# Performance work log

Measured on AMD Instinct MI355X. Metric: run time of the kernel, lower is better.

## Reference

```python
import jax, jax.numpy as jnp
import numpy as np

EPS = 1.0


def _onedirectional_dist(a, b):
    # a: (B, M), b: (B, N) -> per-batch sum over M of min_n (a_m - b_n)^2
    d2 = (a[:, :, None] - b[:, None, :]) ** 2  # (B, M, N)
    return jnp.min(d2, axis=2).sum(axis=1)  # (B,)


def setup_inputs() -> dict:
    key = jax.random.key(0)
    k1, k2, k3 = jax.random.split(key, 3)
    target = jax.random.uniform(k1, (4, 240, 320), dtype=jnp.float32)
    bin_centers = jax.random.uniform(k2, (4, 256), dtype=jnp.float32)
    mask = jax.random.randint(k3, (4, 240, 320), 0, 2).astype(jnp.bool_)
    return {"target": target, "bin_centers": bin_centers, "mask": mask}


def reference(target, bin_centers, mask):
    # masked path of ChamferDistanceLoss.forward
    max_target = jnp.max(jnp.where(mask, target, -jnp.inf))
    max_center = jnp.max(bin_centers)
    mx = jnp.maximum(max_target, max_center)
    mn = jnp.minimum(max_target, max_center)
    pad_value = mx + (mx - mn) + EPS
    B = bin_centers.shape[0]
    # pad bin_centers with one extra column = pad_value
    mod_centers = jnp.concatenate(
        [bin_centers, jnp.broadcast_to(pad_value, (B, 1)).astype(bin_centers.dtype)],
        axis=1,
    )  # (B, n_bins + 1)
    # invalid target pixels replaced by pad_value
    mod_target = jnp.where(mask, target, pad_value).reshape(B, -1)  # (B, H*W)
    bidir = _onedirectional_dist(mod_centers, mod_target) + _onedirectional_dist(
        mod_target, mod_centers
    )
    return jnp.mean(bidir)
```

## Files before the change

### kernel.cpp

```cpp
#include <hip/hip_runtime.h>
#include <math.h>

#define B 4
#define HW 76800
#define NBINS 256
#define TPB 256
#define PXB 1024
#define BPB (HW / PXB)
#define NINT 257
#define KBUK 1024
#define PMW (B * BPB * NINT)
#define TPB2 1024


__device__ __forceinline__ unsigned umaxu(unsigned a, unsigned b) { return a > b ? a : b; }
__device__ __forceinline__ unsigned uminu(unsigned a, unsigned b) { return a < b ? a : b; }

__global__ __launch_bounds__(256) void kmain(const float* __restrict__ target,
                                             const int* __restrict__ mask,
                                             const float* __restrict__ centers,
                                             float* __restrict__ out,
                                             unsigned* __restrict__ ws) {
    __shared__ __align__(16) float s_ct[NBINS];
    __shared__ __align__(16) float s_sc[NBINS];
    __shared__ unsigned short s_tab[KBUK];
    __shared__ unsigned s_M[NINT];
    __shared__ unsigned s_m[NINT];
    __shared__ float s_red[4];
    const int tid = threadIdx.x;
    const int b   = blockIdx.y;
    const int blk = blockIdx.x;

    const float ci = centers[b * NBINS + tid];
    s_ct[tid] = ci;
    s_M[tid]  = 0u;
    s_m[tid]  = 0x7F800000u;
    if (tid == 0) { s_M[256] = 0u; s_m[256] = 0x7F800000u; }
    __syncthreads();

    int rank = 0;
    const float4* c4 = (const float4*)s_ct;
#pragma unroll 8
    for (int g = 0; g < NBINS / 4; ++g) {
        float4 c = c4[g];
        const int j0 = 4 * g;
        rank += (c.x < ci) || (c.x == ci && (j0 + 0) < tid);
        rank += (c.y < ci) || (c.y == ci && (j0 + 1) < tid);
        rank += (c.z < ci) || (c.z == ci && (j0 + 2) < tid);
        rank += (c.w < ci) || (c.w == ci && (j0 + 3) < tid);
    }
    s_sc[rank] = ci;
    __syncthreads();

    {
        const float cr = s_sc[tid];
        const int k0 = (int)(cr * (float)KBUK);
        const int k1 = (tid == NBINS - 1) ? (KBUK - 1)
                                          : (int)(s_sc[tid + 1] * (float)KBUK);
        for (int k = k0 + 1; k <= k1; ++k) s_tab[k] = (unsigned short)(tid + 1);
        if (tid == 0)
            for (int k = 0; k <= k0; ++k) s_tab[k] = 0;
    }
    __syncthreads();

    const int base = b * HW + blk * PXB;
    const float4 p4 = ((const float4*)(target + base))[tid];
    const int4   m4 = ((const int4*)(mask + base))[tid];
    float acc = 0.f;
#pragma unroll
    for (int c = 0; c < 4; ++c) {
        const float p = (c == 0) ? p4.x : (c == 1) ? p4.y : (c == 2) ? p4.z : p4.w;
        const int   m = (c == 0) ? m4.x : (c == 1) ? m4.y : (c == 2) ? m4.z : m4.w;
        int j = s_tab[(int)(p * (float)KBUK)];
        while (j < NBINS && s_sc[j] < p) ++j;
        const float dp = (j > 0)     ? (p - s_sc[j - 1]) : 3e38f;
        const float ds = (j < NBINS) ? (s_sc[j] - p)     : 3e38f;
        if (m) {
            acc += fminf(dp * dp, ds * ds);
            const unsigned pb = __float_as_uint(p);
            atomicMax(&s_M[j], pb);
            atomicMin(&s_m[j], pb);
        }
    }

    for (int o = 32; o > 0; o >>= 1) acc += __shfl_down(acc, o);
    if ((tid & 63) == 0) s_red[tid >> 6] = acc;
    __syncthreads();
    if (tid == 0)
        atomicAdd(out, 0.25f * (s_red[0] + s_red[1] + s_red[2] + s_red[3]));

    unsigned* pM = ws + (size_t)(b * BPB + blk) * NINT;
    unsigned* pm = ws + (size_t)PMW + (size_t)(b * BPB + blk) * NINT;
    pM[tid] = s_M[tid];
    pm[tid] = s_m[tid];
    if (tid == 0) { pM[256] = s_M[256]; pm[256] = s_m[256]; }
}

__global__ __launch_bounds__(1024) void kfold(const float* __restrict__ centers,
                                              const unsigned* __restrict__ ws,
                                              float* __restrict__ out) {
    __shared__ __align__(16) float s_ct[NBINS];
    __shared__ __align__(16) float s_sc[NBINS];
    __shared__ unsigned s_Mp[NINT * 4];
    __shared__ unsigned s_mp[NINT * 4];
    __shared__ float s_P[512];
    __shared__ float s_S[512];
    __shared__ float s_red[4];
    const int tid = threadIdx.x;
    const int b   = blockIdx.x;

    if (tid < NBINS) s_ct[tid] = centers[b * NBINS + tid];
    __syncthreads();
    if (tid < NBINS) {
        const float ci = s_ct[tid];
        int rank = 0;
        const float4* c4 = (const float4*)s_ct;
#pragma unroll 8
        for (int g = 0; g < NBINS / 4; ++g) {
            float4 c = c4[g];
            const int j0 = 4 * g;
            rank += (c.x < ci) || (c.x == ci && (j0 + 0) < tid);
            rank += (c.y < ci) || (c.y == ci && (j0 + 1) < tid);
            rank += (c.z < ci) || (c.z == ci && (j0 + 2) < tid);
            rank += (c.w < ci) || (c.w == ci && (j0 + 3) < tid);
        }
        s_sc[rank] = ci;
    }

    const unsigned* pM = ws + (size_t)b * BPB * NINT;
    const unsigned* pm = ws + (size_t)PMW + (size_t)b * BPB * NINT;
    for (int idx = tid; idx < NINT * 4; idx += TPB2) {
        const int j = idx >> 2, q = idx & 3;
        const int k0 = (q * BPB) / 4, k1 = ((q + 1) * BPB) / 4;
        unsigned Mb = 0u, mb = 0x7F800000u;
        for (int k = k0; k < k1; ++k) {
            Mb = umaxu(Mb, pM[(size_t)k * NINT + j]);
            mb = uminu(mb, pm[(size_t)k * NINT + j]);
        }
        s_Mp[idx] = Mb;
        s_mp[idx] = mb;
    }
    __syncthreads();

    if (tid < 512) {
        if (tid < NINT) {
            unsigned Mb = umaxu(umaxu(s_Mp[4 * tid], s_Mp[4 * tid + 1]),
                                umaxu(s_Mp[4 * tid + 2], s_Mp[4 * tid + 3]));
            unsigned mb = uminu(uminu(s_mp[4 * tid], s_mp[4 * tid + 1]),
                                uminu(s_mp[4 * tid + 2], s_mp[4 * tid + 3]));
            const bool empty = (Mb == 0u) && (mb == 0x7F800000u);
            s_P[tid] = empty ? -3e38f : __uint_as_float(Mb);
            s_S[tid] = empty ?  3e38f : __uint_as_float(mb);
        } else {
            s_P[tid] = -3e38f;
            s_S[tid] =  3e38f;
        }
    }
    __syncthreads();

    for (int s = 1; s < 512; s <<= 1) {
        float pa = 0.f, sa = 0.f;
        if (tid < 512) {
            pa = fmaxf(s_P[tid], (tid >= s) ? s_P[tid - s] : -3e38f);
            sa = fminf(s_S[tid], (tid + s < 512) ? s_S[tid + s] : 3e38f);
        }
        __syncthreads();
        if (tid < 512) { s_P[tid] = pa; s_S[tid] = sa; }
        __syncthreads();
    }

    float d1 = 0.f;
    if (tid < NBINS) {
        const float c = s_sc[tid];
        const float a = c - s_P[tid];
        const float d = s_S[tid + 1] - c;
        d1 = fminf(a * a, d * d);
    }
    for (int o = 32; o > 0; o >>= 1) d1 += __shfl_down(d1, o);
    if ((tid & 63) == 0 && tid < NBINS) s_red[tid >> 6] = d1;
    __syncthreads();
    if (tid == 0)
        atomicAdd(out, 0.25f * (s_red[0] + s_red[1] + s_red[2] + s_red[3]));
}

extern "C" void kernel_launch(void* const* d_in, const int* in_sizes, int n_in,
                              void* d_out, int out_size, void* d_ws, size_t ws_size,
                              hipStream_t stream) {
    const float* target  = (const float*)d_in[0];
    const float* centers = (const float*)d_in[1];
    const int*   mask    = (const int*)d_in[2];
    float* out = (float*)d_out;

    dim3 g1(BPB, B);
    kmain<<<g1, TPB, 0, stream>>>(target, mask, centers, out, (unsigned*)d_ws);
    kfold<<<dim3(B), TPB2, 0, stream>>>(centers, (const unsigned*)d_ws, out);
}
```

Measured before the change: 87.25 us.

## Fuse main and fold kernels into one cooperative launch with grid sync

Merges the per-block histogram kernel and the per-batch fold kernel into a single cooperative kernel that uses a grid-wide sync before one block per batch performs the fold. The fold's parallel Hillis-Steele prefix scan is replaced by a serial per-thread running max/min over the sorted intervals, and the cross-block reduction now runs over all blocks in one pass per thread. This removes a second kernel launch and its dispatch gap, but adds grid-sync overhead across 300 blocks and leaves the fold on four blocks of 256 threads, so it does less parallel work than the 1024-thread fold it replaces.

```diff
diff --git a/kernel.cpp b/kernel.cpp
--- a/kernel.cpp
+++ b/kernel.cpp
@@ -1,5 +1,8 @@
 #include <hip/hip_runtime.h>
+#include <hip/hip_cooperative_groups.h>
 #include <math.h>
+
+namespace cg = cooperative_groups;
 
 #define B 4
 #define HW 76800
@@ -10,22 +13,23 @@
 #define NINT 257
 #define KBUK 1024
 #define PMW (B * BPB * NINT)
-#define TPB2 1024
 
 
 __device__ __forceinline__ unsigned umaxu(unsigned a, unsigned b) { return a > b ? a : b; }
 __device__ __forceinline__ unsigned uminu(unsigned a, unsigned b) { return a < b ? a : b; }
 
-__global__ __launch_bounds__(256) void kmain(const float* __restrict__ target,
-                                             const int* __restrict__ mask,
-                                             const float* __restrict__ centers,
-                                             float* __restrict__ out,
-                                             unsigned* __restrict__ ws) {
+__global__ __launch_bounds__(256) void kchamfer(const float* __restrict__ target,
+                                                const int* __restrict__ mask,
+                                                const float* __restrict__ centers,
+                                                float* __restrict__ out,
+                                                unsigned* __restrict__ ws) {
     __shared__ __align__(16) float s_ct[NBINS];
     __shared__ __align__(16) float s_sc[NBINS];
     __shared__ unsigned short s_tab[KBUK];
     __shared__ unsigned s_M[NINT];
     __shared__ unsigned s_m[NINT];
+    __shared__ float s_P[NINT];
+    __shared__ float s_S[NINT];
     __shared__ float s_red[4];
     const int tid = threadIdx.x;
     const int b   = blockIdx.y;
@@ -94,90 +98,46 @@
     pM[tid] = s_M[tid];
     pm[tid] = s_m[tid];
     if (tid == 0) { pM[256] = s_M[256]; pm[256] = s_m[256]; }
-}
 
-__global__ __launch_bounds__(1024) void kfold(const float* __restrict__ centers,
-                                              const unsigned* __restrict__ ws,
-                                              float* __restrict__ out) {
-    __shared__ __align__(16) float s_ct[NBINS];
-    __shared__ __align__(16) float s_sc[NBINS];
-    __shared__ unsigned s_Mp[NINT * 4];
-    __shared__ unsigned s_mp[NINT * 4];
-    __shared__ float s_P[512];
-    __shared__ float s_S[512];
-    __shared__ float s_red[4];
-    const int tid = threadIdx.x;
-    const int b   = blockIdx.x;
+    __threadfence();
+    cg::this_grid().sync();
+    __threadfence();
 
-    if (tid < NBINS) s_ct[tid] = centers[b * NBINS + tid];
-    __syncthreads();
-    if (tid < NBINS) {
-        const float ci = s_ct[tid];
-        int rank = 0;
-        const float4* c4 = (const float4*)s_ct;
-#pragma unroll 8
-        for (int g = 0; g < NBINS / 4; ++g) {
-            float4 c = c4[g];
-            const int j0 = 4 * g;
-            rank += (c.x < ci) || (c.x == ci && (j0 + 0) < tid);
-            rank += (c.y < ci) || (c.y == ci && (j0 + 1) < tid);
-            rank += (c.z < ci) || (c.z == ci && (j0 + 2) < tid);
-            rank += (c.w < ci) || (c.w == ci && (j0 + 3) < tid);
+    if (blk != 0) return;
+
+    const unsigned* gM = ws + (size_t)b * BPB * NINT;
+    const unsigned* gm = ws + (size_t)PMW + (size_t)b * BPB * NINT;
+    for (int j = tid; j < NINT; j += TPB) {
+        unsigned Mb = 0u, mb = 0x7F800000u;
+#pragma unroll 5
+        for (int k = 0; k < BPB; ++k) {
+            Mb = umaxu(Mb, gM[(size_t)k * NINT + j]);
+            mb = uminu(mb, gm[(size_t)k * NINT + j]);
         }
-        s_sc[rank] = ci;
-    }
-
-    const unsigned* pM = ws + (size_t)b * BPB * NINT;
-    const unsigned* pm = ws + (size_t)PMW + (size_t)b * BPB * NINT;
-    for (int idx = tid; idx < NINT * 4; idx += TPB2) {
-        const int j = idx >> 2, q = idx & 3;
-        const int k0 = (q * BPB) / 4, k1 = ((q + 1) * BPB) / 4;
-        unsigned Mb = 0u, mb = 0x7F800000u;
-        for (int k = k0; k < k1; ++k) {
-            Mb = umaxu(Mb, pM[(size_t)k * NINT + j]);
-            mb = uminu(mb, pm[(size_t)k * NINT + j]);
-        }
-        s_Mp[idx] = Mb;
-        s_mp[idx] = mb;
+        const bool empty = (Mb == 0u) && (mb == 0x7F800000u);
+        s_P[j] = empty ? -3e38f : __uint_as_float(Mb);
+        s_S[j] = empty ?  3e38f : __uint_as_float(mb);
     }
     __syncthreads();
 
-    if (tid < 512) {
-        if (tid < NINT) {
-            unsigned Mb = umaxu(umaxu(s_Mp[4 * tid], s_Mp[4 * tid + 1]),
-                                umaxu(s_Mp[4 * tid + 2], s_Mp[4 * tid + 3]));
-            unsigned mb = uminu(uminu(s_mp[4 * tid], s_mp[4 * tid + 1]),
-                                uminu(s_mp[4 * tid + 2], s_mp[4 * tid + 3]));
-            const bool empty = (Mb == 0u) && (mb == 0x7F800000u);
-            s_P[tid] = empty ? -3e38f : __uint_as_float(Mb);
-            s_S[tid] = empty ?  3e38f : __uint_as_float(mb);
-        } else {
-            s_P[tid] = -3e38f;
-            s_S[tid] =  3e38f;
-        }
+    float runP = -3e38f, myP = -3e38f;
+    for (int j = 0; j < NBINS; ++j) {
+        runP = fmaxf(runP, s_P[j]);
+        if (j == tid) myP = runP;
     }
-    __syncthreads();
-
-    for (int s = 1; s < 512; s <<= 1) {
-        float pa = 0.f, sa = 0.f;
-        if (tid < 512) {
-            pa = fmaxf(s_P[tid], (tid >= s) ? s_P[tid - s] : -3e38f);
-            sa = fminf(s_S[tid], (tid + s < 512) ? s_S[tid + s] : 3e38f);
-        }
-        __syncthreads();
-        if (tid < 512) { s_P[tid] = pa; s_S[tid] = sa; }
-        __syncthreads();
+    float runS = 3e38f, myS = 3e38f;
+    for (int j = NINT - 1; j >= 1; --j) {
+        runS = fminf(runS, s_S[j]);
+        if (j == tid + 1) myS = runS;
     }
 
-    float d1 = 0.f;
-    if (tid < NBINS) {
-        const float c = s_sc[tid];
-        const float a = c - s_P[tid];
-        const float d = s_S[tid + 1] - c;
-        d1 = fminf(a * a, d * d);
-    }
+    const float c = s_sc[tid];
+    const float a = c - myP;
+    const float d = myS - c;
+    float d1 = fminf(a * a, d * d);
     for (int o = 32; o > 0; o >>= 1) d1 += __shfl_down(d1, o);
-    if ((tid & 63) == 0 && tid < NBINS) s_red[tid >> 6] = d1;
+    __syncthreads();
+    if ((tid & 63) == 0) s_red[tid >> 6] = d1;
     __syncthreads();
     if (tid == 0)
         atomicAdd(out, 0.25f * (s_red[0] + s_red[1] + s_red[2] + s_red[3]));
@@ -189,9 +149,13 @@
     const float* target  = (const float*)d_in[0];
     const float* centers = (const float*)d_in[1];
     const int*   mask    = (const int*)d_in[2];
-    float* out = (float*)d_out;
+    float*       out     = (float*)d_out;
+    unsigned*    ws      = (unsigned*)d_ws;
 
-    dim3 g1(BPB, B);
-    kmain<<<g1, TPB, 0, stream>>>(target, mask, centers, out, (unsigned*)d_ws);
-    kfold<<<dim3(B), TPB2, 0, stream>>>(centers, (const unsigned*)d_ws, out);
+    void* args[] = {(void*)&target, (void*)&mask, (void*)&centers,
+                    (void*)&out, (void*)&ws};
+    dim3 grid(BPB, B);
+    dim3 blk(TPB);
+    hipLaunchCooperativeKernel(reinterpret_cast<void*>(kchamfer),
+                               grid, blk, args, 0, stream);
 }
```

Measured after the change: 167.2 us. 1.92x slower.
